# Optimization experiments

Hardware: AMD Instinct MI355X
Metric: run time of the kernel (lower is better)

## Reference

```python
import jax, jax.numpy as jnp
import numpy as np

B, S, IN_DIM = 8, 4096, 1024
H, D = 16, 64          # num_heads, head_dim (attention_dim = H*D = 1024)
OUT_DIM = 1024
EPS = 1e-6
HI = jax.lax.Precision.HIGHEST


def setup_inputs() -> dict:
    key = jax.random.key(0)
    ks = jax.random.split(key, 9)
    sx = 1.0 / np.sqrt(IN_DIM)
    so = 1.0 / np.sqrt(H * D)
    return {
        "x":  jax.random.normal(ks[0], (B, S, IN_DIM), jnp.float32),
        "wq": jax.random.normal(ks[1], (IN_DIM, H, D), jnp.float32) * sx,
        "bq": jnp.zeros((H, D), jnp.float32),
        "wk": jax.random.normal(ks[2], (IN_DIM, H, D), jnp.float32) * sx,
        "bk": jnp.zeros((H, D), jnp.float32),
        "wv": jax.random.normal(ks[3], (IN_DIM, H, D), jnp.float32) * sx,
        "bv": jnp.zeros((H, D), jnp.float32),
        "wo": jax.random.normal(ks[4], (H, D, OUT_DIM), jnp.float32) * so,
        "bo": jnp.zeros((OUT_DIM,), jnp.float32),
    }


def _feature_map(t):
    return jax.nn.elu(t) + 1.0


def reference(x, wq, bq, wk, bk, wv, bv, wo, bo):
    # QKV projections: [B,S,IN] x [IN,H,D] -> [B,S,H,D]
    q = jnp.einsum('bsi,ihd->bshd', x, wq) + bq
    k = jnp.einsum('bsi,ihd->bshd', x, wk) + bk
    v = jnp.einsum('bsi,ihd->bshd', x, wv) + bv

    Q = _feature_map(q)
    K = _feature_map(k)

    # Faithful to source: KV is an elementwise K*V reduced over seq -> [B,H,D]
    KV = jnp.einsum('bshd,bshd->bhd', K, v, precision=HI)
    Ksum = jnp.sum(K, axis=1)                      # [B,H,D]
    Z = 1.0 / (Q * Ksum[:, None, :, :] + EPS)      # [B,S,H,D]
    attn = Q * KV[:, None, :, :] * Z               # [B,S,H,D]

    # output projection contracts heads and head_dim
    out = jnp.einsum('bshd,hdo->bso', attn, wo) + bo
    return jax.nn.gelu(out)  # flax default gelu is approximate=True
```

## Files before the change

kernel.cpp:

```cpp
#include <hip/hip_runtime.h>


#define SEQ   4096
#define MROWS 32768
#define KDIM  1024
#define HD    1024

typedef __bf16 bf16x8 __attribute__((ext_vector_type(8)));
typedef float floatx4 __attribute__((ext_vector_type(4)));

__device__ __forceinline__ unsigned short f2bf(float f) {
    unsigned int u = __float_as_uint(f);
    u += 0x7fffu + ((u >> 16) & 1u);
    return (unsigned short)(u >> 16);
}
__device__ __forceinline__ void cvt8(const float* __restrict__ p, unsigned short* d) {
    const float4 a = *(const float4*)p;
    const float4 b = *(const float4*)(p + 4);
    d[0] = f2bf(a.x); d[1] = f2bf(a.y); d[2] = f2bf(a.z); d[3] = f2bf(a.w);
    d[4] = f2bf(b.x); d[5] = f2bf(b.y); d[6] = f2bf(b.z); d[7] = f2bf(b.w);
}

typedef const __attribute__((address_space(1))) unsigned int* gas_t;
typedef __attribute__((address_space(3))) unsigned int* las_t;
__device__ __forceinline__ void async16(const void* g, void* l) {
    __builtin_amdgcn_global_load_lds((gas_t)g, (las_t)l, 16, 0, 0);
}

__global__ __launch_bounds__(256)
void cvt_x(const float* __restrict__ x, unsigned short* __restrict__ xb)
{
    const size_t p = ((size_t)blockIdx.x * 256 + threadIdx.x) * 8;
    union { uint4 u; unsigned short s[8]; } o;
    cvt8(x + p, o.s);
    *(uint4*)(xb + p) = o.u;
}

__global__ __launch_bounds__(256)
void transpose_w(const float* __restrict__ wk, const float* __restrict__ wv,
                 unsigned short* __restrict__ wkT, unsigned short* __restrict__ wvT)
{
    __shared__ alignas(16) unsigned short Ts[64][72];
    const float* W = blockIdx.z ? wv : wk;
    unsigned short* WT = blockIdx.z ? wvT : wkT;
    const int k0 = blockIdx.x * 64, n0 = blockIdx.y * 64;
    const int t = threadIdx.x;
    const int r4 = (t >> 4) * 4, c4 = (t & 15) * 4;
#pragma unroll
    for (int i = 0; i < 4; i++) {
        const float4 f = *(const float4*)(W + (size_t)(k0 + r4 + i) * HD + n0 + c4);
        Ts[c4 + 0][r4 + i] = f2bf(f.x);
        Ts[c4 + 1][r4 + i] = f2bf(f.y);
        Ts[c4 + 2][r4 + i] = f2bf(f.z);
        Ts[c4 + 3][r4 + i] = f2bf(f.w);
    }
    __syncthreads();
    const int rr = t >> 3, cc = (t & 7) * 8;
#pragma unroll
    for (int h = 0; h < 2; h++)
        *(uint4*)(WT + (size_t)(n0 + rr + h * 32) * KDIM + k0 + cc) =
            *(const uint4*)&Ts[rr + h * 32][cc];
}

__global__ __launch_bounds__(512, 2)
void kv_gemm_fast(const unsigned short* __restrict__ xb,
                  const unsigned short* __restrict__ wkT,
                  const unsigned short* __restrict__ wvT,
                  const float* __restrict__ bk, const float* __restrict__ bv,
                  float2* __restrict__ KVZ)
{
    __shared__ alignas(16) unsigned short As[2][256 * 64];
    __shared__ alignas(16) unsigned short Bks[2][128 * 64];
    __shared__ alignas(16) unsigned short Bvs[2][128 * 64];

    const int t = threadIdx.x;

    const int id = blockIdx.x;
    const int xcd = id & 7, o = id >> 3;
    const int mtile = xcd * 16 + (o >> 3);
    const int ntile = o & 7;
    const int m0 = mtile * 256;
    const int n0 = ntile * 128;
    const int b  = m0 >> 12;

    const int w = t >> 6, lane = t & 63;
    const int wm = w >> 1, wn = w & 1;
    const int lrow = lane & 15, quad = lane >> 4;
    const int swz = lane & 7;

    const int srow  = t >> 3;
    const int sunit = (t & 7) ^ (srow & 7);
    const unsigned short* gA = xb  + (size_t)(m0 + srow) * KDIM + sunit * 8;
    const unsigned short* gK = wkT + (size_t)(n0 + srow) * KDIM + sunit * 8;
    const unsigned short* gV = wvT + (size_t)(n0 + srow) * KDIM + sunit * 8;

#define STAGE(c, tk) do {                                                     \
        const int koff_ = (tk) * 64;                                          \
        async16(gA + koff_,                    &As[c][         t * 8]);       \
        async16(gA + koff_ +  64 * KDIM,       &As[c][ 4096 +  t * 8]);       \
        async16(gA + koff_ + 128 * KDIM,       &As[c][ 8192 +  t * 8]);       \
        async16(gA + koff_ + 192 * KDIM,       &As[c][12288 +  t * 8]);       \
        async16(gK + koff_,                    &Bks[c][        t * 8]);       \
        async16(gK + koff_ +  64 * KDIM,       &Bks[c][4096 +  t * 8]);       \
        async16(gV + koff_,                    &Bvs[c][        t * 8]);       \
        async16(gV + koff_ +  64 * KDIM,       &Bvs[c][4096 +  t * 8]);       \
    } while (0)

    STAGE(0, 0);
    STAGE(1, 1);

    floatx4 accK[4][4], accV[4][4];
#pragma unroll
    for (int i = 0; i < 4; i++)
#pragma unroll
        for (int j = 0; j < 4; j++) {
            accK[i][j] = (floatx4){0.f, 0.f, 0.f, 0.f};
            accV[i][j] = (floatx4){0.f, 0.f, 0.f, 0.f};
        }

    asm volatile("s_waitcnt vmcnt(8)" ::: "memory");
    __builtin_amdgcn_s_barrier();

    for (int tk = 0; tk < 16; ++tk) {
        const int c = tk & 1;
        const unsigned short* A  = As[c];
        const unsigned short* BK = Bks[c];
        const unsigned short* BV = Bvs[c];

#pragma unroll
        for (int kk = 0; kk < 2; ++kk) {
            bf16x8 af[4];
#pragma unroll
            for (int mi = 0; mi < 4; ++mi) {
                const int row = wm * 64 + mi * 16 + lrow;
                af[mi] = *(const bf16x8*)&A[row * 64 + (((kk * 4 + quad) ^ swz) << 3)];
            }
#pragma unroll
            for (int mat = 0; mat < 2; ++mat) {
                const unsigned short* Bp = mat ? BV : BK;
                bf16x8 bf[4];
#pragma unroll
                for (int ni = 0; ni < 4; ++ni) {
                    const int row = wn * 64 + ni * 16 + lrow;
                    bf[ni] = *(const bf16x8*)&Bp[row * 64 + (((kk * 4 + quad) ^ swz) << 3)];
                }
                __builtin_amdgcn_s_barrier();
                __builtin_amdgcn_s_setprio(1);
                if (mat == 0) {
#pragma unroll
                    for (int mi = 0; mi < 4; ++mi)
#pragma unroll
                        for (int ni = 0; ni < 4; ++ni)
                            accK[mi][ni] = __builtin_amdgcn_mfma_f32_16x16x32_bf16(
                                af[mi], bf[ni], accK[mi][ni], 0, 0, 0);
                } else {
#pragma unroll
                    for (int mi = 0; mi < 4; ++mi)
#pragma unroll
                        for (int ni = 0; ni < 4; ++ni)
                            accV[mi][ni] = __builtin_amdgcn_mfma_f32_16x16x32_bf16(
                                af[mi], bf[ni], accV[mi][ni], 0, 0, 0);
                }
                __builtin_amdgcn_s_setprio(0);
            }
        }

        __builtin_amdgcn_s_barrier();
        if (tk + 2 < 16) {
            STAGE(c, tk + 2);
            asm volatile("s_waitcnt vmcnt(8)" ::: "memory");
        } else {
            asm volatile("s_waitcnt vmcnt(0)" ::: "memory");
        }
        __builtin_amdgcn_s_barrier();
    }
#undef STAGE

#pragma unroll
    for (int ni = 0; ni < 4; ++ni) {
        const int colw = n0 + wn * 64 + ni * 16 + lrow;
        const float bkf = bk[colw];
        const float bvf = bv[colw];
        float pKV = 0.f, pK = 0.f;
#pragma unroll
        for (int mi = 0; mi < 4; ++mi) {
#pragma unroll
            for (int r = 0; r < 4; ++r) {
                const float kv = accK[mi][ni][r] + bkf;
                const float K  = (kv > 0.f) ? (kv + 1.f) : __expf(kv);
                const float vv = accV[mi][ni][r] + bvf;
                pKV += K * vv;
                pK  += K;
            }
        }
        pKV += __shfl_xor(pKV, 16, 64);
        pKV += __shfl_xor(pKV, 32, 64);
        pK  += __shfl_xor(pK, 16, 64);
        pK  += __shfl_xor(pK, 32, 64);
        if (quad == 0) {
            atomicAdd(&KVZ[b * HD + colw].x, pKV);
            atomicAdd(&KVZ[b * HD + colw].y, pK);
        }
    }
}

__global__ __launch_bounds__(256)
void kv_gemm(const float* __restrict__ x,
             const float* __restrict__ wk, const float* __restrict__ bk,
             const float* __restrict__ wv, const float* __restrict__ bv,
             float2* __restrict__ KVZ)
{
    __shared__ alignas(16) unsigned short As [128][40];
    __shared__ alignas(16) unsigned short BsK[128][40];
    __shared__ alignas(16) unsigned short BsV[128][40];

    const int t = threadIdx.x;
    const int n0 = blockIdx.x * 128;
    const int m0 = blockIdx.y * 128;
    const int b  = m0 >> 12;

    const int wave = t >> 6, lane = t & 63;
    const int wm = wave >> 1, wn = wave & 1;
    const int lrow = lane & 15, quad = lane >> 4;

    floatx4 accK[4][4], accV[4][4];
#pragma unroll
    for (int i = 0; i < 4; i++)
#pragma unroll
        for (int j = 0; j < 4; j++) {
            accK[i][j] = (floatx4){0.f, 0.f, 0.f, 0.f};
            accV[i][j] = (floatx4){0.f, 0.f, 0.f, 0.f};
        }

    const int arow0 = t >> 2, akc = (t & 3) * 8;
    const int bk0 = t >> 4, bnc = (t & 15) * 8;

    for (int k0 = 0; k0 < KDIM; k0 += 32) {
        __syncthreads();
        {
            union { uint4 u; unsigned short s[8]; } ua, ub;
            cvt8(x + (size_t)(m0 + arow0) * KDIM + k0 + akc, ua.s);
            cvt8(x + (size_t)(m0 + arow0 + 64) * KDIM + k0 + akc, ub.s);
            *(uint4*)&As[arow0][akc] = ua.u;
            *(uint4*)&As[arow0 + 64][akc] = ub.u;
        }
        {
            unsigned short k0s[8], k1s[8], v0s[8], v1s[8];
            cvt8(wk + (size_t)(k0 + bk0) * HD + n0 + bnc, k0s);
            cvt8(wk + (size_t)(k0 + bk0 + 16) * HD + n0 + bnc, k1s);
            cvt8(wv + (size_t)(k0 + bk0) * HD + n0 + bnc, v0s);
            cvt8(wv + (size_t)(k0 + bk0 + 16) * HD + n0 + bnc, v1s);
#pragma unroll
            for (int j = 0; j < 8; j++) {
                BsK[bnc + j][bk0]      = k0s[j];
                BsK[bnc + j][bk0 + 16] = k1s[j];
                BsV[bnc + j][bk0]      = v0s[j];
                BsV[bnc + j][bk0 + 16] = v1s[j];
            }
        }
        __syncthreads();

        bf16x8 af[4], bfK[4], bfV[4];
#pragma unroll
        for (int mi = 0; mi < 4; mi++)
            af[mi] = *(const bf16x8*)&As[wm * 64 + mi * 16 + lrow][quad * 8];
#pragma unroll
        for (int ni = 0; ni < 4; ni++) {
            bfK[ni] = *(const bf16x8*)&BsK[wn * 64 + ni * 16 + lrow][quad * 8];
            bfV[ni] = *(const bf16x8*)&BsV[wn * 64 + ni * 16 + lrow][quad * 8];
        }
#pragma unroll
        for (int mi = 0; mi < 4; mi++)
#pragma unroll
            for (int ni = 0; ni < 4; ni++) {
                accK[mi][ni] = __builtin_amdgcn_mfma_f32_16x16x32_bf16(
                    af[mi], bfK[ni], accK[mi][ni], 0, 0, 0);
                accV[mi][ni] = __builtin_amdgcn_mfma_f32_16x16x32_bf16(
                    af[mi], bfV[ni], accV[mi][ni], 0, 0, 0);
            }
    }

#pragma unroll
    for (int ni = 0; ni < 4; ni++) {
        const int colw = n0 + wn * 64 + ni * 16 + lrow;
        const float bkf = bk[colw];
        const float bvf = bv[colw];
        float pKV = 0.f, pK = 0.f;
#pragma unroll
        for (int mi = 0; mi < 4; mi++) {
#pragma unroll
            for (int r = 0; r < 4; r++) {
                const float kk = accK[mi][ni][r] + bkf;
                const float K  = (kk > 0.f) ? (kk + 1.f) : __expf(kk);
                const float vv = accV[mi][ni][r] + bvf;
                pKV += K * vv;
                pK  += K;
            }
        }
        pKV += __shfl_xor(pKV, 16, 64);
        pKV += __shfl_xor(pKV, 32, 64);
        pK  += __shfl_xor(pK, 16, 64);
        pK  += __shfl_xor(pK, 32, 64);
        if (quad == 0) {
            atomicAdd(&KVZ[b * HD + colw].x, pKV);
            atomicAdd(&KVZ[b * HD + colw].y, pK);
        }
    }
}

__global__ __launch_bounds__(256)
void rowgemm(const float2* __restrict__ KVZ,
             const float* __restrict__ wo, const float* __restrict__ bo,
             float* __restrict__ rowf)
{
    __shared__ float a[1024];
    __shared__ float red[4][64];
    const int t = threadIdx.x;
    const int b = blockIdx.x;
    const int o0 = blockIdx.y * 64;

    for (int c = t; c < 1024; c += 256) {
        const float2 z = KVZ[b * HD + c];
        a[c] = z.x / z.y;
    }
    __syncthreads();

    const int cs = t >> 6, oi = t & 63;
    float p = 0.f;
    const int cbeg = cs * 256;
    for (int c = cbeg; c < cbeg + 256; ++c)
        p += a[c] * wo[(size_t)c * HD + o0 + oi];
    red[cs][oi] = p;
    __syncthreads();

    if (t < 64) {
        float v = red[0][t] + red[1][t] + red[2][t] + red[3][t] + bo[o0 + t];
        const float g = 0.5f * v *
            (1.f + tanhf(0.7978845608028654f * (v + 0.044715f * v * v * v)));
        rowf[b * HD + o0 + t] = g;
    }
}

__global__ __launch_bounds__(256)
void broadcast_rows(const float* __restrict__ rowf, float* __restrict__ out)
{
    const size_t idx = (size_t)blockIdx.x * 256 + threadIdx.x;
    const size_t p = idx * 4;
    const int row = (int)(p >> 10);
    const int b = row >> 12;
    const int col = (int)(p & 1023);
    *(float4*)(out + p) = *(const float4*)(rowf + b * HD + col);
}

extern "C" void kernel_launch(void* const* d_in, const int* in_sizes, int n_in,
                              void* d_out, int out_size, void* d_ws, size_t ws_size,
                              hipStream_t stream)
{
    const float* x  = (const float*)d_in[0];
    const float* wk = (const float*)d_in[3];
    const float* bk = (const float*)d_in[4];
    const float* wv = (const float*)d_in[5];
    const float* bv = (const float*)d_in[6];
    const float* wo = (const float*)d_in[7];
    const float* bo = (const float*)d_in[8];
    float* out = (float*)d_out;

    const size_t NEED = (size_t)72 * 1024 * 1024;
    if (ws_size >= NEED) {
        unsigned short* xb  = (unsigned short*)d_ws;
        unsigned short* wkT = (unsigned short*)((char*)d_ws + (67u << 20));
        unsigned short* wvT = (unsigned short*)((char*)d_ws + (69u << 20));
        float2* KVZ = (float2*)((char*)d_ws + (71u << 20));
        float* rowf = (float*)((char*)d_ws + (71u << 20) + 65536);

        hipMemsetAsync(KVZ, 0, 8 * HD * sizeof(float2), stream);
        cvt_x<<<dim3(MROWS * KDIM / 8 / 256), 256, 0, stream>>>(x, xb);
        transpose_w<<<dim3(16, 16, 2), 256, 0, stream>>>(wk, wv, wkT, wvT);
        kv_gemm_fast<<<dim3(1024), 512, 0, stream>>>(xb, wkT, wvT, bk, bv, KVZ);
        rowgemm<<<dim3(8, 16), 256, 0, stream>>>(KVZ, wo, bo, rowf);
        broadcast_rows<<<dim3((MROWS * HD / 4) / 256), 256, 0, stream>>>(rowf, out);
    } else {
        float2* KVZ = (float2*)d_ws;
        float* rowf = (float*)((char*)d_ws + 65536);
        hipMemsetAsync(KVZ, 0, 8 * HD * sizeof(float2), stream);
        kv_gemm<<<dim3(8, 256), 256, 0, stream>>>(x, wk, bk, wv, bv, KVZ);
        rowgemm<<<dim3(8, 16), 256, 0, stream>>>(KVZ, wo, bo, rowf);
        broadcast_rows<<<dim3((MROWS * HD / 4) / 256), 256, 0, stream>>>(rowf, out);
    }
}
```

Baseline: 418.3 us.

## Deepen KV GEMM pipeline to 4 stages and fuse row GEMM with broadcast

The KV GEMM now uses a 4-buffer ring of 32-wide K tiles with three tiles prefetched. K and V MFMAs are interleaved and the intra-tile barriers are dropped, aiming to hide load latency better. The launch bound drops to one block per SM. The output row GEMM plus GELU is fused with the broadcast write, removing a kernel launch and the intermediate buffer at the cost of recomputing the small row GEMM per sequence chunk.

```diff
diff --git a/kernel.cpp b/kernel.cpp
--- a/kernel.cpp
+++ b/kernel.cpp
@@ -5,6 +5,7 @@
 #define MROWS 32768
 #define KDIM  1024
 #define HD    1024
+#define T32   32
 
 typedef __bf16 bf16x8 __attribute__((ext_vector_type(8)));
 typedef float floatx4 __attribute__((ext_vector_type(4)));
@@ -62,16 +63,15 @@
             *(const uint4*)&Ts[rr + h * 32][cc];
 }
 
-__global__ __launch_bounds__(512, 2)
+__global__ __launch_bounds__(512, 1)
 void kv_gemm_fast(const unsigned short* __restrict__ xb,
                   const unsigned short* __restrict__ wkT,
                   const unsigned short* __restrict__ wvT,
                   const float* __restrict__ bk, const float* __restrict__ bv,
                   float2* __restrict__ KVZ)
 {
-    __shared__ alignas(16) unsigned short As[2][256 * 64];
-    __shared__ alignas(16) unsigned short Bks[2][128 * 64];
-    __shared__ alignas(16) unsigned short Bvs[2][128 * 64];
+    __shared__ alignas(16) unsigned short As[4][256 * 32];
+    __shared__ alignas(16) unsigned short Bs[4][256 * 32];
 
     const int t = threadIdx.x;
 
@@ -86,28 +86,27 @@
     const int w = t >> 6, lane = t & 63;
     const int wm = w >> 1, wn = w & 1;
     const int lrow = lane & 15, quad = lane >> 4;
-    const int swz = lane & 7;
-
-    const int srow  = t >> 3;
-    const int sunit = (t & 7) ^ (srow & 7);
-    const unsigned short* gA = xb  + (size_t)(m0 + srow) * KDIM + sunit * 8;
-    const unsigned short* gK = wkT + (size_t)(n0 + srow) * KDIM + sunit * 8;
-    const unsigned short* gV = wvT + (size_t)(n0 + srow) * KDIM + sunit * 8;
+
+    const int usw = quad ^ ((lrow >> 1) & 3);
+
+    const int srow  = t >> 2;
+    const int usrc  = (t & 3) ^ ((t >> 3) & 3);
+    const unsigned short* gA0 = xb  + (size_t)(m0 + srow) * KDIM + usrc * 8;
+    const unsigned short* gA1 = gA0 + (size_t)128 * KDIM;
+    const unsigned short* gBk = wkT + (size_t)(n0 + srow) * KDIM + usrc * 8;
+    const unsigned short* gBv = wvT + (size_t)(n0 + srow) * KDIM + usrc * 8;
 
 #define STAGE(c, tk) do {                                                     \
-        const int koff_ = (tk) * 64;                                          \
-        async16(gA + koff_,                    &As[c][         t * 8]);       \
-        async16(gA + koff_ +  64 * KDIM,       &As[c][ 4096 +  t * 8]);       \
-        async16(gA + koff_ + 128 * KDIM,       &As[c][ 8192 +  t * 8]);       \
-        async16(gA + koff_ + 192 * KDIM,       &As[c][12288 +  t * 8]);       \
-        async16(gK + koff_,                    &Bks[c][        t * 8]);       \
-        async16(gK + koff_ +  64 * KDIM,       &Bks[c][4096 +  t * 8]);       \
-        async16(gV + koff_,                    &Bvs[c][        t * 8]);       \
-        async16(gV + koff_ +  64 * KDIM,       &Bvs[c][4096 +  t * 8]);       \
+        const int ko_ = (tk) * 32;                                            \
+        async16(gA0 + ko_, &As[c][(0 * 512 + t) * 8]);                        \
+        async16(gA1 + ko_, &As[c][(1 * 512 + t) * 8]);                        \
+        async16(gBk + ko_, &Bs[c][(0 * 512 + t) * 8]);                        \
+        async16(gBv + ko_, &Bs[c][(1 * 512 + t) * 8]);                        \
     } while (0)
 
     STAGE(0, 0);
     STAGE(1, 1);
+    STAGE(2, 2);
 
     floatx4 accK[4][4], accV[4][4];
 #pragma unroll
@@ -121,55 +120,39 @@
     asm volatile("s_waitcnt vmcnt(8)" ::: "memory");
     __builtin_amdgcn_s_barrier();
 
-    for (int tk = 0; tk < 16; ++tk) {
-        const int c = tk & 1;
-        const unsigned short* A  = As[c];
-        const unsigned short* BK = Bks[c];
-        const unsigned short* BV = Bvs[c];
-
-#pragma unroll
-        for (int kk = 0; kk < 2; ++kk) {
-            bf16x8 af[4];
-#pragma unroll
-            for (int mi = 0; mi < 4; ++mi) {
-                const int row = wm * 64 + mi * 16 + lrow;
-                af[mi] = *(const bf16x8*)&A[row * 64 + (((kk * 4 + quad) ^ swz) << 3)];
+    for (int tk = 0; tk < T32; ++tk) {
+        const unsigned short* A = As[tk & 3];
+        const unsigned short* B = Bs[tk & 3];
+
+        bf16x8 af[4], bK[4], bV[4];
+#pragma unroll
+        for (int mi = 0; mi < 4; ++mi)
+            af[mi] = *(const bf16x8*)&A[(wm * 64 + mi * 16 + lrow) * 32 + usw * 8];
+#pragma unroll
+        for (int ni = 0; ni < 4; ++ni) {
+            const int br = wn * 64 + ni * 16 + lrow;
+            bK[ni] = *(const bf16x8*)&B[ br        * 32 + usw * 8];
+            bV[ni] = *(const bf16x8*)&B[(br + 128) * 32 + usw * 8];
+        }
+
+        __builtin_amdgcn_s_setprio(1);
+#pragma unroll
+        for (int mi = 0; mi < 4; ++mi)
+#pragma unroll
+            for (int ni = 0; ni < 4; ++ni) {
+                accK[mi][ni] = __builtin_amdgcn_mfma_f32_16x16x32_bf16(
+                    af[mi], bK[ni], accK[mi][ni], 0, 0, 0);
+                accV[mi][ni] = __builtin_amdgcn_mfma_f32_16x16x32_bf16(
+                    af[mi], bV[ni], accV[mi][ni], 0, 0, 0);
             }
-#pragma unroll
-            for (int mat = 0; mat < 2; ++mat) {
-                const unsigned short* Bp = mat ? BV : BK;
-                bf16x8 bf[4];
-#pragma unroll
-                for (int ni = 0; ni < 4; ++ni) {
-                    const int row = wn * 64 + ni * 16 + lrow;
-                    bf[ni] = *(const bf16x8*)&Bp[row * 64 + (((kk * 4 + quad) ^ swz) << 3)];
-                }
-                __builtin_amdgcn_s_barrier();
-                __builtin_amdgcn_s_setprio(1);
-                if (mat == 0) {
-#pragma unroll
-                    for (int mi = 0; mi < 4; ++mi)
-#pragma unroll
-                        for (int ni = 0; ni < 4; ++ni)
-                            accK[mi][ni] = __builtin_amdgcn_mfma_f32_16x16x32_bf16(
-                                af[mi], bf[ni], accK[mi][ni], 0, 0, 0);
-                } else {
-#pragma unroll
-                    for (int mi = 0; mi < 4; ++mi)
-#pragma unroll
-                        for (int ni = 0; ni < 4; ++ni)
-                            accV[mi][ni] = __builtin_amdgcn_mfma_f32_16x16x32_bf16(
-                                af[mi], bf[ni], accV[mi][ni], 0, 0, 0);
-                }
-                __builtin_amdgcn_s_setprio(0);
-            }
-        }
-
-        __builtin_amdgcn_s_barrier();
-        if (tk + 2 < 16) {
-            STAGE(c, tk + 2);
+        __builtin_amdgcn_s_setprio(0);
+
+        if (tk + 3 < T32) {
+            STAGE((tk + 3) & 3, tk + 3);
             asm volatile("s_waitcnt vmcnt(8)" ::: "memory");
-        } else {
+        } else if (tk == T32 - 3) {
+            asm volatile("s_waitcnt vmcnt(4)" ::: "memory");
+        } else if (tk == T32 - 2) {
             asm volatile("s_waitcnt vmcnt(0)" ::: "memory");
         }
         __builtin_amdgcn_s_barrier();
@@ -186,8 +169,8 @@
         for (int mi = 0; mi < 4; ++mi) {
 #pragma unroll
             for (int r = 0; r < 4; ++r) {
-                const float kv = accK[mi][ni][r] + bkf;
-                const float K  = (kv > 0.f) ? (kv + 1.f) : __expf(kv);
+                const float kk = accK[mi][ni][r] + bkf;
+                const float K  = (kk > 0.f) ? (kk + 1.f) : __expf(kk);
                 const float vv = accV[mi][ni][r] + bvf;
                 pKV += K * vv;
                 pK  += K;
@@ -309,6 +292,45 @@
 }
 
 __global__ __launch_bounds__(256)
+void rowgemm_bcast(const float2* __restrict__ KVZ,
+                   const float* __restrict__ wo, const float* __restrict__ bo,
+                   float* __restrict__ out)
+{
+    __shared__ float a[1024];
+    __shared__ float red[4][64];
+    __shared__ float sval[64];
+    const int t = threadIdx.x;
+    const int b = blockIdx.x;
+    const int o0 = blockIdx.y * 64;
+    const int s0 = blockIdx.z * 512;
+
+    for (int c = t; c < 1024; c += 256) {
+        const float2 z = KVZ[b * HD + c];
+        a[c] = z.x / z.y;
+    }
+    __syncthreads();
+
+    const int cs = t >> 6, oi = t & 63;
+    float p = 0.f;
+    const int cbeg = cs * 256;
+    for (int c = cbeg; c < cbeg + 256; ++c)
+        p += a[c] * wo[(size_t)c * HD + o0 + oi];
+    red[cs][oi] = p;
+    __syncthreads();
+
+    if (t < 64) {
+        float v = red[0][t] + red[1][t] + red[2][t] + red[3][t] + bo[o0 + t];
+        sval[t] = 0.5f * v *
+            (1.f + tanhf(0.7978845608028654f * (v + 0.044715f * v * v * v)));
+    }
+    __syncthreads();
+
+    const float4 sv4 = *(const float4*)&sval[(t & 15) * 4];
+    for (int r = t >> 4; r < 512; r += 16)
+        *(float4*)&out[((size_t)(b * SEQ + s0 + r)) * HD + o0 + (t & 15) * 4] = sv4;
+}
+
+__global__ __launch_bounds__(256)
 void rowgemm(const float2* __restrict__ KVZ,
              const float* __restrict__ wo, const float* __restrict__ bo,
              float* __restrict__ rowf)
@@ -371,14 +393,12 @@
         unsigned short* wkT = (unsigned short*)((char*)d_ws + (67u << 20));
         unsigned short* wvT = (unsigned short*)((char*)d_ws + (69u << 20));
         float2* KVZ = (float2*)((char*)d_ws + (71u << 20));
-        float* rowf = (float*)((char*)d_ws + (71u << 20) + 65536);
 
         hipMemsetAsync(KVZ, 0, 8 * HD * sizeof(float2), stream);
         cvt_x<<<dim3(MROWS * KDIM / 8 / 256), 256, 0, stream>>>(x, xb);
         transpose_w<<<dim3(16, 16, 2), 256, 0, stream>>>(wk, wv, wkT, wvT);
         kv_gemm_fast<<<dim3(1024), 512, 0, stream>>>(xb, wkT, wvT, bk, bv, KVZ);
-        rowgemm<<<dim3(8, 16), 256, 0, stream>>>(KVZ, wo, bo, rowf);
-        broadcast_rows<<<dim3((MROWS * HD / 4) / 256), 256, 0, stream>>>(rowf, out);
+        rowgemm_bcast<<<dim3(8, 16, 8), 256, 0, stream>>>(KVZ, wo, bo, out);
     } else {
         float2* KVZ = (float2*)d_ws;
         float* rowf = (float*)((char*)d_ws + 65536);
```

Result: faster. 408.9 us (-2.3%).
